# Kernel optimization log

Measured on AMD Instinct MI355X. Metric: run time of the kernel, lower is better.

The kernel has to match this reference:

```python
import jax, jax.numpy as jnp
import numpy as np

N = 50000   # nodes
E = 500000  # edges
G = 64      # graphs in batch
H = 2       # attention heads
D = 64      # hidden per head (hid)
F_IN = 4    # num_features
C = 5       # num_classes
NEG_SLOPE = 0.2


def setup_inputs() -> dict:
    key = jax.random.key(0)
    ks = jax.random.split(key, 24)
    inp = {
        'x': jax.random.normal(ks[0], (N, F_IN), jnp.float32),
        'edge_index': jax.random.randint(ks[1], (2, E), 0, N, dtype=jnp.int64),
        'batch': jnp.sort(jax.random.randint(ks[2], (N,), 0, G, dtype=jnp.int64)),
    }
    ins = [F_IN, H * D, H * D, H * D]
    ki = 3
    for l, fin in enumerate(ins, 1):
        s = 1.0 / np.sqrt(fin)
        inp[f'W{l}'] = s * jax.random.normal(ks[ki], (fin, H * D), jnp.float32); ki += 1
        inp[f'asrc{l}'] = 0.1 * jax.random.normal(ks[ki], (H, D), jnp.float32); ki += 1
        inp[f'adst{l}'] = 0.1 * jax.random.normal(ks[ki], (H, D), jnp.float32); ki += 1
        inp[f'b{l}'] = 0.01 * jax.random.normal(ks[ki], (H * D,), jnp.float32); ki += 1
    inp['lin_w'] = (1.0 / np.sqrt(H * D)) * jax.random.normal(ks[ki], (H * D, C), jnp.float32); ki += 1
    inp['lin_b'] = jnp.zeros((C,), jnp.float32)
    return inp


def gat_conv(x, src, dst, W, a_src, a_dst, b):
    # x: [N, Fin] -> h: [N, H, D]
    h = (x @ W).reshape(-1, H, D)
    alpha_src = jnp.sum(h * a_src, axis=-1)  # [N, H]
    alpha_dst = jnp.sum(h * a_dst, axis=-1)  # [N, H]
    e = jax.nn.leaky_relu(alpha_src[src] + alpha_dst[dst], NEG_SLOPE)  # [E, H]
    # segment softmax over incoming edges of each dst node
    e_max = jax.ops.segment_max(e, dst, num_segments=N)  # [N, H]
    e_exp = jnp.exp(e - e_max[dst])
    denom = jax.ops.segment_sum(e_exp, dst, num_segments=N)
    alpha = e_exp / (denom[dst] + 1e-16)  # [E, H]
    msg = h[src] * alpha[:, :, None]  # [E, H, D]
    out = jax.ops.segment_sum(msg, dst, num_segments=N)  # [N, H, D]
    return out.reshape(-1, H * D) + b


def reference(x, edge_index, batch,
              W1, asrc1, adst1, b1,
              W2, asrc2, adst2, b2,
              W3, asrc3, adst3, b3,
              W4, asrc4, adst4, b4,
              lin_w, lin_b):
    src, dst = edge_index[0], edge_index[1]
    h = jax.nn.relu(gat_conv(x, src, dst, W1, asrc1, adst1, b1))
    h = jax.nn.relu(gat_conv(h, src, dst, W2, asrc2, adst2, b2))
    h = jax.nn.relu(gat_conv(h, src, dst, W3, asrc3, adst3, b3))
    h = jax.nn.relu(gat_conv(h, src, dst, W4, asrc4, adst4, b4))
    # global mean pool over graphs
    sums = jax.ops.segment_sum(h, batch, num_segments=G)  # [G, 128]
    counts = jax.ops.segment_sum(jnp.ones((h.shape[0],), h.dtype), batch, num_segments=G)
    pooled = sums / jnp.maximum(counts, 1.0)[:, None]
    return jax.nn.sigmoid(pooled @ lin_w + lin_b)  # [G, C]
```

## Files before the change

kernel.cpp:

```cpp
#include <hip/hip_runtime.h>
#include <math.h>

#define NHEAD 2
#define NDIM  64
#define HD    128
#define NGRAPH 64
#define NCLS  5
#define NEG_SLOPE 0.2f

typedef __attribute__((ext_vector_type(8))) short bf16x8;
typedef __attribute__((ext_vector_type(4))) float f32x4;

static __device__ __forceinline__ unsigned short f2bf(float f) {
    unsigned int u = __float_as_uint(f);
    u = (u + 0x7fff + ((u >> 16) & 1)) >> 16;
    return (unsigned short)u;
}
static __device__ __forceinline__ float bf2f(unsigned short b) {
    return __uint_as_float((unsigned int)b << 16);
}


__global__ void k_deg(const int* __restrict__ dst, int* __restrict__ deg, int E) {
    int i = blockIdx.x * blockDim.x + threadIdx.x;
    if (i < E) atomicAdd(&deg[dst[i]], 1);
}

__global__ __launch_bounds__(256) void k_scan_local(const int* __restrict__ deg,
                                                    int* __restrict__ ptr,
                                                    int* __restrict__ bsum, int n) {
    __shared__ int wsum[4];
    const int tid = threadIdx.x, lane = tid & 63, wid = tid >> 6;
    const int base = blockIdx.x * 2048 + tid * 8;
    int v[8];
    #pragma unroll
    for (int k = 0; k < 8; ++k) {
        int i = base + k;
        v[k] = (i < n) ? deg[i] : 0;
    }
    #pragma unroll
    for (int k = 1; k < 8; ++k) v[k] += v[k - 1];
    int x = v[7];
    #pragma unroll
    for (int off = 1; off < 64; off <<= 1) {
        int t = __shfl_up(x, off, 64);
        if (lane >= off) x += t;
    }
    if (lane == 63) wsum[wid] = x;
    __syncthreads();
    int woff = 0;
    #pragma unroll
    for (int k = 0; k < 4; ++k) woff += (k < wid) ? wsum[k] : 0;
    int texcl = woff + x - v[7];
    #pragma unroll
    for (int k = 0; k < 8; ++k) {
        int i = base + k;
        if (i < n) ptr[i + 1] = texcl + v[k];
    }
    if (tid == 255) bsum[blockIdx.x] = woff + x;
    if (blockIdx.x == 0 && tid == 0) ptr[0] = 0;
}

__global__ void k_scan_bsum(int* __restrict__ bsum, int B) {
    int lane = threadIdx.x;
    int carry = 0;
    for (int base = 0; base < B; base += 64) {
        int i = base + lane;
        int v = (i < B) ? bsum[i] : 0;
        int x = v;
        #pragma unroll
        for (int off = 1; off < 64; off <<= 1) {
            int t = __shfl_up(x, off, 64);
            if (lane >= off) x += t;
        }
        if (i < B) bsum[i] = carry + x - v;
        carry += __shfl(x, 63, 64);
    }
}

__global__ __launch_bounds__(256) void k_scan_add(int* __restrict__ ptr,
                                                  const int* __restrict__ bsum, int n) {
    int off = bsum[blockIdx.x];
    if (off == 0) return;
    const int base = blockIdx.x * 2048 + threadIdx.x * 8;
    #pragma unroll
    for (int k = 0; k < 8; ++k) {
        int i = base + k;
        if (i < n) ptr[i + 1] += off;
    }
}

__global__ void k_scatter(const int* __restrict__ src, const int* __restrict__ dst,
                          const int* __restrict__ ptr, int* __restrict__ fill,
                          int* __restrict__ csr, int E) {
    int i = blockIdx.x * blockDim.x + threadIdx.x;
    if (i < E) {
        int d = dst[i];
        int pos = atomicAdd(&fill[d], 1);
        csr[ptr[d] + pos] = src[i];
    }
}


__global__ void k_prepw(const float* __restrict__ W2, const float* __restrict__ W3,
                        const float* __restrict__ W4, unsigned short* __restrict__ Wt) {
    int idx = blockIdx.x * blockDim.x + threadIdx.x;
    if (idx >= 3 * HD * HD) return;
    int l = idx / (HD * HD), rem = idx % (HD * HD);
    int n = rem >> 7, k = rem & 127;
    const float* W = (l == 0) ? W2 : (l == 1) ? W3 : W4;
    Wt[idx] = f2bf(W[k * HD + n]);
}

__global__ void k_gemm1_alpha(const float* __restrict__ x, const float* __restrict__ W,
                              const float* __restrict__ asrc, const float* __restrict__ adst,
                              unsigned short* __restrict__ out, float* __restrict__ oas,
                              float* __restrict__ oad, int N) {
    int n = (blockIdx.x * blockDim.x + threadIdx.x) >> 6;
    int lane = threadIdx.x & 63;
    if (n >= N) return;
    float4 xv = *(const float4*)&x[n * 4];
    int c0 = lane * 2;
    float2 w0 = *(const float2*)&W[c0];
    float2 w1 = *(const float2*)&W[128 + c0];
    float2 w2 = *(const float2*)&W[256 + c0];
    float2 w3 = *(const float2*)&W[384 + c0];
    float v0 = xv.x * w0.x + xv.y * w1.x + xv.z * w2.x + xv.w * w3.x;
    float v1 = xv.x * w0.y + xv.y * w1.y + xv.z * w2.y + xv.w * w3.y;
    unsigned short b0 = f2bf(v0), b1 = f2bf(v1);
    unsigned int packed = (unsigned int)b0 | ((unsigned int)b1 << 16);
    *(unsigned int*)&out[(size_t)n * HD + c0] = packed;
    float vx = bf2f(b0), vy = bf2f(b1);
    float2 av = *(const float2*)&asrc[c0];
    float2 dv = *(const float2*)&adst[c0];
    float s = vx * av.x + vy * av.y;
    float t = vx * dv.x + vy * dv.y;
    #pragma unroll
    for (int off = 16; off > 0; off >>= 1) {
        s += __shfl_xor(s, off);
        t += __shfl_xor(t, off);
    }
    if ((lane & 31) == 0) {
        int head = lane >> 5;
        oas[n * 2 + head] = s;
        oad[n * 2 + head] = t;
    }
}

__global__ __launch_bounds__(256) void k_gemm_mfma(const unsigned short* __restrict__ A,
                                                   const unsigned short* __restrict__ Wt,
                                                   const float* __restrict__ asrc,
                                                   const float* __restrict__ adst,
                                                   unsigned short* __restrict__ out,
                                                   float* __restrict__ oas,
                                                   float* __restrict__ oad, int N) {
    const int tid = threadIdx.x;
    const int nbase = blockIdx.x * 64;
    const int lane = tid & 63, w = tid >> 6;
    const int l15 = lane & 15, quad = lane >> 4;
    const int koff = quad * 8;

    float av[8], dv[8];
    #pragma unroll
    for (int c = 0; c < 8; ++c) {
        av[c] = asrc[c * 16 + l15];
        dv[c] = adst[c * 16 + l15];
    }

    f32x4 acc[8];
    #pragma unroll
    for (int c = 0; c < 8; ++c) acc[c] = (f32x4)(0.f);

    const int g0 = nbase + w * 16 + l15;
    #pragma unroll
    for (int ks = 0; ks < 4; ++ks) {
        bf16x8 a0 = (bf16x8)(short)0;
        if (g0 < N) a0 = *(const bf16x8*)&A[(size_t)g0 * HD + ks * 32 + koff];
        #pragma unroll
        for (int c = 0; c < 8; ++c) {
            bf16x8 b = *(const bf16x8*)&Wt[(size_t)(c * 16 + l15) * HD + ks * 32 + koff];
            acc[c] = __builtin_amdgcn_mfma_f32_16x16x32_bf16(a0, b, acc[c], 0, 0, 0);
        }
    }

    const int rowb = nbase + w * 16 + quad * 4;
    #pragma unroll
    for (int c = 0; c < 8; ++c) {
        f32x4 v = acc[c];
        int col = c * 16 + l15;
        #pragma unroll
        for (int r = 0; r < 4; ++r) {
            int row = rowb + r;
            if (row < N) out[(size_t)row * HD + col] = f2bf(v[r]);
        }
    }
    #pragma unroll
    for (int r = 0; r < 4; ++r) {
        float ps0 = 0.f, ps1 = 0.f, pd0 = 0.f, pd1 = 0.f;
        #pragma unroll
        for (int c = 0; c < 4; ++c) {
            float hv = acc[c][r];
            ps0 += hv * av[c]; pd0 += hv * dv[c];
        }
        #pragma unroll
        for (int c = 4; c < 8; ++c) {
            float hv = acc[c][r];
            ps1 += hv * av[c]; pd1 += hv * dv[c];
        }
        #pragma unroll
        for (int off = 1; off < 16; off <<= 1) {
            ps0 += __shfl_xor(ps0, off);
            ps1 += __shfl_xor(ps1, off);
            pd0 += __shfl_xor(pd0, off);
            pd1 += __shfl_xor(pd1, off);
        }
        int row = rowb + r;
        if (l15 == 0 && row < N) {
            *(float2*)&oas[row * 2] = make_float2(ps0, ps1);
            *(float2*)&oad[row * 2] = make_float2(pd0, pd1);
        }
    }
}

__global__ __launch_bounds__(256) void k_agg(const unsigned short* __restrict__ h,
                                             const float* __restrict__ oas,
                                             const float* __restrict__ oad,
                                             const int* __restrict__ ptr,
                                             const int* __restrict__ csr,
                                             const float* __restrict__ bias,
                                             unsigned short* __restrict__ out, int N) {
    const int tid = threadIdx.x;
    const int lane = tid & 63;
    const int grp = lane >> 4, sub = lane & 15;
    const int gbase = lane & 48;
    const int n = ((blockIdx.x * blockDim.x + tid) >> 6) * 4 + grp;
    const int hsel = sub >> 3;
    const bool valid = (n < N);

    int beg = 0, end = 0;
    float2 adn = make_float2(0.f, 0.f);
    if (valid) {
        beg = ptr[n]; end = ptr[n + 1];
        adn = *(const float2*)&oad[n * 2];
    }
    float m0 = -INFINITY, m1 = -INFINITY, l0 = 0.f, l1 = 0.f;
    float acc[8];
    #pragma unroll
    for (int k = 0; k < 8; ++k) acc[k] = 0.f;

    auto accum = [&](uint4 hv, float pj) {
        #pragma unroll
        for (int k = 0; k < 4; ++k) {
            unsigned int u = (&hv.x)[k];
            acc[2 * k]     += pj * __uint_as_float(u << 16);
            acc[2 * k + 1] += pj * __uint_as_float(u & 0xffff0000u);
        }
    };

    int cbeg = beg;
    while (__any(cbeg < end)) {
        int rem = end - cbeg;
        int cnt = rem < 0 ? 0 : (rem > 16 ? 16 : rem);
        int s = 0;
        float e0 = -INFINITY, e1 = -INFINITY;
        if (sub < cnt) {
            s = csr[cbeg + sub];
            float2 as = *(const float2*)&oas[s * 2];
            e0 = as.x + adn.x; e0 = (e0 >= 0.f) ? e0 : NEG_SLOPE * e0;
            e1 = as.y + adn.y; e1 = (e1 >= 0.f) ? e1 : NEG_SLOPE * e1;
        }
        float c0 = e0, c1 = e1;
        #pragma unroll
        for (int off = 8; off > 0; off >>= 1) {
            c0 = fmaxf(c0, __shfl_xor(c0, off));
            c1 = fmaxf(c1, __shfl_xor(c1, off));
        }
        float nm0 = fmaxf(m0, c0), nm1 = fmaxf(m1, c1);
        float sc0 = (nm0 == -INFINITY) ? 0.f : __expf(m0 - nm0);
        float sc1 = (nm1 == -INFINITY) ? 0.f : __expf(m1 - nm1);
        float p0 = (sub < cnt) ? __expf(e0 - nm0) : 0.f;
        float p1 = (sub < cnt) ? __expf(e1 - nm1) : 0.f;
        float s0 = p0, s1 = p1;
        #pragma unroll
        for (int off = 8; off > 0; off >>= 1) {
            s0 += __shfl_xor(s0, off);
            s1 += __shfl_xor(s1, off);
        }
        l0 = l0 * sc0 + s0;
        l1 = l1 * sc1 + s1;
        m0 = nm0; m1 = nm1;
        float scl = hsel ? sc1 : sc0;
        #pragma unroll
        for (int k = 0; k < 8; ++k) acc[k] *= scl;

        int jm = cnt;
        jm = max(jm, __shfl_xor(jm, 16));
        jm = max(jm, __shfl_xor(jm, 32));

        auto fetchp = [&](int j, uint4& hv, float& pj) {
            int sj = __shfl(s, gbase + j);
            float pa = __shfl(p0, gbase + j);
            float pb = __shfl(p1, gbase + j);
            pj = hsel ? pb : pa;
            hv = make_uint4(0, 0, 0, 0);
            if (j < cnt)
                hv = *(const uint4*)&h[(size_t)sj * HD + sub * 8];
        };
        uint4 hA, hB = make_uint4(0, 0, 0, 0);
        float pA, pB = 0.f;
        fetchp(0, hA, pA);
        if (jm > 1) fetchp(1, hB, pB);
        for (int j = 2; j < jm; ++j) {
            uint4 hC; float pC;
            fetchp(j, hC, pC);
            accum(hA, pA);
            hA = hB; pA = pB;
            hB = hC; pB = pC;
        }
        accum(hA, pA);
        if (jm > 1) accum(hB, pB);

        cbeg += 16;
    }

    if (valid) {
        float lsel = hsel ? l1 : l0;
        float inv = 1.f / (lsel + 1e-16f);
        float4 ba = *(const float4*)&bias[sub * 8];
        float4 bb = *(const float4*)&bias[sub * 8 + 4];
        float o[8];
        o[0] = fmaxf(acc[0] * inv + ba.x, 0.f);
        o[1] = fmaxf(acc[1] * inv + ba.y, 0.f);
        o[2] = fmaxf(acc[2] * inv + ba.z, 0.f);
        o[3] = fmaxf(acc[3] * inv + ba.w, 0.f);
        o[4] = fmaxf(acc[4] * inv + bb.x, 0.f);
        o[5] = fmaxf(acc[5] * inv + bb.y, 0.f);
        o[6] = fmaxf(acc[6] * inv + bb.z, 0.f);
        o[7] = fmaxf(acc[7] * inv + bb.w, 0.f);
        uint4 pk;
        pk.x = (unsigned int)f2bf(o[0]) | ((unsigned int)f2bf(o[1]) << 16);
        pk.y = (unsigned int)f2bf(o[2]) | ((unsigned int)f2bf(o[3]) << 16);
        pk.z = (unsigned int)f2bf(o[4]) | ((unsigned int)f2bf(o[5]) << 16);
        pk.w = (unsigned int)f2bf(o[6]) | ((unsigned int)f2bf(o[7]) << 16);
        *(uint4*)&out[(size_t)n * HD + sub * 8] = pk;
    }
}

__global__ void k_pool(const unsigned short* __restrict__ feat, const int* __restrict__ batch,
                       float* __restrict__ pooled, int* __restrict__ gcount, int N) {
    int col = threadIdx.x;
    int n0 = blockIdx.x * 128;
    int n1 = min(n0 + 128, N);
    float acc = 0.f;
    int curg = -1, runlen = 0;
    for (int n = n0; n < n1; ++n) {
        int g = batch[n];
        if (g != curg) {
            if (curg >= 0) {
                atomicAdd(&pooled[curg * HD + col], acc);
                if (col == 0) atomicAdd(&gcount[curg], runlen);
            }
            acc = 0.f; runlen = 0;
            curg = g;
        }
        acc += bf2f(feat[(size_t)n * HD + col]);
        runlen++;
    }
    if (curg >= 0) {
        atomicAdd(&pooled[curg * HD + col], acc);
        if (col == 0) atomicAdd(&gcount[curg], runlen);
    }
}

__global__ void k_final(const float* __restrict__ pooled, const int* __restrict__ gcount,
                        const float* __restrict__ lw, const float* __restrict__ lb,
                        float* __restrict__ out) {
    int tid = threadIdx.x;
    if (tid >= NGRAPH * NCLS) return;
    int g = tid / NCLS, c = tid % NCLS;
    float cnt = fmaxf((float)gcount[g], 1.f);
    const float* p = pooled + g * HD;
    float sum = 0.f;
    for (int k = 0; k < HD; ++k)
        sum += p[k] * lw[k * NCLS + c];
    float z = lb[c] + sum / cnt;
    out[tid] = 1.f / (1.f + __expf(-z));
}


static inline size_t al256(size_t x) { return (x + 255) & ~(size_t)255; }

extern "C" void kernel_launch(void* const* d_in, const int* in_sizes, int n_in,
                              void* d_out, int out_size, void* d_ws, size_t ws_size,
                              hipStream_t stream) {
    const int N = in_sizes[0] / 4;
    const int E = in_sizes[1] / 2;

    const float* x     = (const float*)d_in[0];
    const int*   esrc  = (const int*)d_in[1];
    const int*   edst  = esrc + E;
    const int*   batch = (const int*)d_in[2];
    const float* Wl[4]  = {(const float*)d_in[3],  (const float*)d_in[7],
                           (const float*)d_in[11], (const float*)d_in[15]};
    const float* asr[4] = {(const float*)d_in[4],  (const float*)d_in[8],
                           (const float*)d_in[12], (const float*)d_in[16]};
    const float* ads[4] = {(const float*)d_in[5],  (const float*)d_in[9],
                           (const float*)d_in[13], (const float*)d_in[17]};
    const float* bs[4]  = {(const float*)d_in[6],  (const float*)d_in[10],
                           (const float*)d_in[14], (const float*)d_in[18]};
    const float* lin_w = (const float*)d_in[19];
    const float* lin_b = (const float*)d_in[20];
    float* out = (float*)d_out;

    char* w = (char*)d_ws;
    size_t off = 0;
    auto alloc = [&](size_t bytes) -> void* {
        void* p = w + off;
        off = al256(off + bytes);
        return p;
    };
    int*   deg    = (int*)alloc((size_t)N * 4);
    int*   fill   = (int*)alloc((size_t)N * 4);
    int*   gcount = (int*)alloc((size_t)NGRAPH * 4);
    float* pooled = (float*)alloc((size_t)NGRAPH * HD * 4);
    size_t zbytes = off;
    int*   ptr    = (int*)alloc((size_t)(N + 1) * 4);
    int*   bsum   = (int*)alloc((size_t)1024 * 4);
    int*   csr    = (int*)alloc((size_t)E * 4);
    unsigned short* hbuf = (unsigned short*)alloc((size_t)N * HD * 2);
    unsigned short* feat = (unsigned short*)alloc((size_t)N * HD * 2);
    unsigned short* Wt   = (unsigned short*)alloc((size_t)3 * HD * HD * 2);
    float* a_src  = (float*)alloc((size_t)N * 2 * 4);
    float* a_dst  = (float*)alloc((size_t)N * 2 * 4);
    (void)ws_size; (void)n_in; (void)out_size;

    hipMemsetAsync(d_ws, 0, zbytes, stream);

    k_prepw<<<(3 * HD * HD + 255) / 256, 256, 0, stream>>>(Wl[1], Wl[2], Wl[3], Wt);
    k_deg<<<(E + 255) / 256, 256, 0, stream>>>(edst, deg, E);
    const int SB = (N + 2047) / 2048;
    k_scan_local<<<SB, 256, 0, stream>>>(deg, ptr, bsum, N);
    k_scan_bsum<<<1, 64, 0, stream>>>(bsum, SB);
    k_scan_add<<<SB, 256, 0, stream>>>(ptr, bsum, N);
    k_scatter<<<(E + 255) / 256, 256, 0, stream>>>(esrc, edst, ptr, fill, csr, E);

    const int node_wave_blocks = (N + 3) / 4;
    const int agg_blocks = (N + 15) / 16;

    for (int layer = 0; layer < 4; ++layer) {
        if (layer == 0) {
            k_gemm1_alpha<<<node_wave_blocks, 256, 0, stream>>>(
                x, Wl[0], asr[0], ads[0], hbuf, a_src, a_dst, N);
        } else {
            k_gemm_mfma<<<(N + 63) / 64, 256, 0, stream>>>(
                feat, Wt + (size_t)(layer - 1) * HD * HD,
                asr[layer], ads[layer], hbuf, a_src, a_dst, N);
        }
        k_agg<<<agg_blocks, 256, 0, stream>>>(hbuf, a_src, a_dst, ptr, csr, bs[layer], feat, N);
    }

    k_pool<<<(N + 127) / 128, 128, 0, stream>>>(feat, batch, pooled, gcount, N);
    k_final<<<1, 320, 0, stream>>>(pooled, gcount, lin_w, lin_b, out);
}
```

Baseline: 396.1 us.

## Fuse GAT aggregation with next layer's MFMA projection via LDS tile

Merges each layer's edge aggregation kernel with the following layer's bf16 MFMA projection and attention-logit computation. Aggregated rows are staged in a padded shared-memory tile instead of being written to and re-read from global memory. Ping-pong buffers for h and the alpha arrays keep reads and writes apart across layers. This removes three kernel launches and the intermediate feature round trip, but each block now runs 4 sequential aggregation passes before its GEMM, which lowers parallelism in the gather phase.

```diff
diff --git a/kernel.cpp b/kernel.cpp
--- a/kernel.cpp
+++ b/kernel.cpp
@@ -7,6 +7,7 @@
 #define NGRAPH 64
 #define NCLS  5
 #define NEG_SLOPE 0.2f
+#define LDA 136
 
 typedef __attribute__((ext_vector_type(8))) short bf16x8;
 typedef __attribute__((ext_vector_type(4))) float f32x4;
@@ -147,96 +148,12 @@
     }
 }
 
-__global__ __launch_bounds__(256) void k_gemm_mfma(const unsigned short* __restrict__ A,
-                                                   const unsigned short* __restrict__ Wt,
-                                                   const float* __restrict__ asrc,
-                                                   const float* __restrict__ adst,
-                                                   unsigned short* __restrict__ out,
-                                                   float* __restrict__ oas,
-                                                   float* __restrict__ oad, int N) {
-    const int tid = threadIdx.x;
-    const int nbase = blockIdx.x * 64;
-    const int lane = tid & 63, w = tid >> 6;
-    const int l15 = lane & 15, quad = lane >> 4;
-    const int koff = quad * 8;
-
-    float av[8], dv[8];
-    #pragma unroll
-    for (int c = 0; c < 8; ++c) {
-        av[c] = asrc[c * 16 + l15];
-        dv[c] = adst[c * 16 + l15];
-    }
-
-    f32x4 acc[8];
-    #pragma unroll
-    for (int c = 0; c < 8; ++c) acc[c] = (f32x4)(0.f);
-
-    const int g0 = nbase + w * 16 + l15;
-    #pragma unroll
-    for (int ks = 0; ks < 4; ++ks) {
-        bf16x8 a0 = (bf16x8)(short)0;
-        if (g0 < N) a0 = *(const bf16x8*)&A[(size_t)g0 * HD + ks * 32 + koff];
-        #pragma unroll
-        for (int c = 0; c < 8; ++c) {
-            bf16x8 b = *(const bf16x8*)&Wt[(size_t)(c * 16 + l15) * HD + ks * 32 + koff];
-            acc[c] = __builtin_amdgcn_mfma_f32_16x16x32_bf16(a0, b, acc[c], 0, 0, 0);
-        }
-    }
-
-    const int rowb = nbase + w * 16 + quad * 4;
-    #pragma unroll
-    for (int c = 0; c < 8; ++c) {
-        f32x4 v = acc[c];
-        int col = c * 16 + l15;
-        #pragma unroll
-        for (int r = 0; r < 4; ++r) {
-            int row = rowb + r;
-            if (row < N) out[(size_t)row * HD + col] = f2bf(v[r]);
-        }
-    }
-    #pragma unroll
-    for (int r = 0; r < 4; ++r) {
-        float ps0 = 0.f, ps1 = 0.f, pd0 = 0.f, pd1 = 0.f;
-        #pragma unroll
-        for (int c = 0; c < 4; ++c) {
-            float hv = acc[c][r];
-            ps0 += hv * av[c]; pd0 += hv * dv[c];
-        }
-        #pragma unroll
-        for (int c = 4; c < 8; ++c) {
-            float hv = acc[c][r];
-            ps1 += hv * av[c]; pd1 += hv * dv[c];
-        }
-        #pragma unroll
-        for (int off = 1; off < 16; off <<= 1) {
-            ps0 += __shfl_xor(ps0, off);
-            ps1 += __shfl_xor(ps1, off);
-            pd0 += __shfl_xor(pd0, off);
-            pd1 += __shfl_xor(pd1, off);
-        }
-        int row = rowb + r;
-        if (l15 == 0 && row < N) {
-            *(float2*)&oas[row * 2] = make_float2(ps0, ps1);
-            *(float2*)&oad[row * 2] = make_float2(pd0, pd1);
-        }
-    }
-}
-
-__global__ __launch_bounds__(256) void k_agg(const unsigned short* __restrict__ h,
-                                             const float* __restrict__ oas,
-                                             const float* __restrict__ oad,
-                                             const int* __restrict__ ptr,
-                                             const int* __restrict__ csr,
-                                             const float* __restrict__ bias,
-                                             unsigned short* __restrict__ out, int N) {
-    const int tid = threadIdx.x;
-    const int lane = tid & 63;
-    const int grp = lane >> 4, sub = lane & 15;
-    const int gbase = lane & 48;
-    const int n = ((blockIdx.x * blockDim.x + tid) >> 6) * 4 + grp;
-    const int hsel = sub >> 3;
+static __device__ __forceinline__ uint4 agg_row(
+    const unsigned short* __restrict__ h, const float* __restrict__ oas,
+    const float* __restrict__ oad, const int* __restrict__ ptr,
+    const int* __restrict__ csr, const float* __restrict__ bias,
+    int n, int N, int sub, int gbase, int hsel) {
     const bool valid = (n < N);
-
     int beg = 0, end = 0;
     float2 adn = make_float2(0.f, 0.f);
     if (valid) {
@@ -323,6 +240,7 @@
         cbeg += 16;
     }
 
+    uint4 pk = make_uint4(0, 0, 0, 0);
     if (valid) {
         float lsel = hsel ? l1 : l0;
         float inv = 1.f / (lsel + 1e-16f);
@@ -337,13 +255,113 @@
         o[5] = fmaxf(acc[5] * inv + bb.y, 0.f);
         o[6] = fmaxf(acc[6] * inv + bb.z, 0.f);
         o[7] = fmaxf(acc[7] * inv + bb.w, 0.f);
-        uint4 pk;
         pk.x = (unsigned int)f2bf(o[0]) | ((unsigned int)f2bf(o[1]) << 16);
         pk.y = (unsigned int)f2bf(o[2]) | ((unsigned int)f2bf(o[3]) << 16);
         pk.z = (unsigned int)f2bf(o[4]) | ((unsigned int)f2bf(o[5]) << 16);
         pk.w = (unsigned int)f2bf(o[6]) | ((unsigned int)f2bf(o[7]) << 16);
-        *(uint4*)&out[(size_t)n * HD + sub * 8] = pk;
-    }
+    }
+    return pk;
+}
+
+__global__ __launch_bounds__(256) void k_agg_gemm(
+    const unsigned short* __restrict__ hin,
+    const float* __restrict__ oas_in, const float* __restrict__ oad_in,
+    const int* __restrict__ ptr, const int* __restrict__ csr,
+    const float* __restrict__ bias,
+    const unsigned short* __restrict__ Wt,
+    const float* __restrict__ asrc, const float* __restrict__ adst,
+    unsigned short* __restrict__ hout,
+    float* __restrict__ oas_out, float* __restrict__ oad_out, int N) {
+    __shared__ unsigned short As[64 * LDA];
+    const int tid = threadIdx.x;
+    const int lane = tid & 63, w = tid >> 6;
+    const int grp = lane >> 4, sub = lane & 15;
+    const int gbase = lane & 48;
+    const int hsel = sub >> 3;
+    const int nbase = blockIdx.x * 64;
+
+    #pragma unroll 1
+    for (int p = 0; p < 4; ++p) {
+        const int row = w * 16 + p * 4 + grp;
+        uint4 pk = agg_row(hin, oas_in, oad_in, ptr, csr, bias,
+                           nbase + row, N, sub, gbase, hsel);
+        *(uint4*)&As[(size_t)row * LDA + sub * 8] = pk;
+    }
+    __syncthreads();
+
+    float av[8], dv[8];
+    #pragma unroll
+    for (int c = 0; c < 8; ++c) {
+        av[c] = asrc[c * 16 + sub];
+        dv[c] = adst[c * 16 + sub];
+    }
+    f32x4 acc[8];
+    #pragma unroll
+    for (int c = 0; c < 8; ++c) acc[c] = (f32x4)(0.f);
+
+    #pragma unroll
+    for (int ks = 0; ks < 4; ++ks) {
+        bf16x8 a0 = *(const bf16x8*)&As[(size_t)(w * 16 + sub) * LDA + ks * 32 + grp * 8];
+        #pragma unroll
+        for (int c = 0; c < 8; ++c) {
+            bf16x8 b = *(const bf16x8*)&Wt[(size_t)(c * 16 + sub) * HD + ks * 32 + grp * 8];
+            acc[c] = __builtin_amdgcn_mfma_f32_16x16x32_bf16(a0, b, acc[c], 0, 0, 0);
+        }
+    }
+
+    const int rowb = nbase + w * 16 + grp * 4;
+    #pragma unroll
+    for (int c = 0; c < 8; ++c) {
+        f32x4 v = acc[c];
+        int col = c * 16 + sub;
+        #pragma unroll
+        for (int r = 0; r < 4; ++r) {
+            int row = rowb + r;
+            if (row < N) hout[(size_t)row * HD + col] = f2bf(v[r]);
+        }
+    }
+    #pragma unroll
+    for (int r = 0; r < 4; ++r) {
+        float ps0 = 0.f, ps1 = 0.f, pd0 = 0.f, pd1 = 0.f;
+        #pragma unroll
+        for (int c = 0; c < 4; ++c) {
+            float hv = acc[c][r];
+            ps0 += hv * av[c]; pd0 += hv * dv[c];
+        }
+        #pragma unroll
+        for (int c = 4; c < 8; ++c) {
+            float hv = acc[c][r];
+            ps1 += hv * av[c]; pd1 += hv * dv[c];
+        }
+        #pragma unroll
+        for (int off = 1; off < 16; off <<= 1) {
+            ps0 += __shfl_xor(ps0, off);
+            ps1 += __shfl_xor(ps1, off);
+            pd0 += __shfl_xor(pd0, off);
+            pd1 += __shfl_xor(pd1, off);
+        }
+        int row = rowb + r;
+        if (sub == 0 && row < N) {
+            *(float2*)&oas_out[row * 2] = make_float2(ps0, ps1);
+            *(float2*)&oad_out[row * 2] = make_float2(pd0, pd1);
+        }
+    }
+}
+
+__global__ __launch_bounds__(256) void k_agg_final(
+    const unsigned short* __restrict__ hin,
+    const float* __restrict__ oas_in, const float* __restrict__ oad_in,
+    const int* __restrict__ ptr, const int* __restrict__ csr,
+    const float* __restrict__ bias,
+    unsigned short* __restrict__ out, int N) {
+    const int tid = threadIdx.x;
+    const int lane = tid & 63;
+    const int grp = lane >> 4, sub = lane & 15;
+    const int gbase = lane & 48;
+    const int hsel = sub >> 3;
+    const int n = ((blockIdx.x * blockDim.x + tid) >> 6) * 4 + grp;
+    uint4 pk = agg_row(hin, oas_in, oad_in, ptr, csr, bias, n, N, sub, gbase, hsel);
+    if (n < N) *(uint4*)&out[(size_t)n * HD + sub * 8] = pk;
 }
 
 __global__ void k_pool(const unsigned short* __restrict__ feat, const int* __restrict__ batch,
@@ -427,11 +445,14 @@
     int*   ptr    = (int*)alloc((size_t)(N + 1) * 4);
     int*   bsum   = (int*)alloc((size_t)1024 * 4);
     int*   csr    = (int*)alloc((size_t)E * 4);
-    unsigned short* hbuf = (unsigned short*)alloc((size_t)N * HD * 2);
+    unsigned short* hA   = (unsigned short*)alloc((size_t)N * HD * 2);
+    unsigned short* hB   = (unsigned short*)alloc((size_t)N * HD * 2);
     unsigned short* feat = (unsigned short*)alloc((size_t)N * HD * 2);
     unsigned short* Wt   = (unsigned short*)alloc((size_t)3 * HD * HD * 2);
-    float* a_src  = (float*)alloc((size_t)N * 2 * 4);
-    float* a_dst  = (float*)alloc((size_t)N * 2 * 4);
+    float* asA = (float*)alloc((size_t)N * 2 * 4);
+    float* adA = (float*)alloc((size_t)N * 2 * 4);
+    float* asB = (float*)alloc((size_t)N * 2 * 4);
+    float* adB = (float*)alloc((size_t)N * 2 * 4);
     (void)ws_size; (void)n_in; (void)out_size;
 
     hipMemsetAsync(d_ws, 0, zbytes, stream);
@@ -444,20 +465,21 @@
     k_scan_add<<<SB, 256, 0, stream>>>(ptr, bsum, N);
     k_scatter<<<(E + 255) / 256, 256, 0, stream>>>(esrc, edst, ptr, fill, csr, E);
 
-    const int node_wave_blocks = (N + 3) / 4;
-    const int agg_blocks = (N + 15) / 16;
-
-    for (int layer = 0; layer < 4; ++layer) {
-        if (layer == 0) {
-            k_gemm1_alpha<<<node_wave_blocks, 256, 0, stream>>>(
-                x, Wl[0], asr[0], ads[0], hbuf, a_src, a_dst, N);
-        } else {
-            k_gemm_mfma<<<(N + 63) / 64, 256, 0, stream>>>(
-                feat, Wt + (size_t)(layer - 1) * HD * HD,
-                asr[layer], ads[layer], hbuf, a_src, a_dst, N);
-        }
-        k_agg<<<agg_blocks, 256, 0, stream>>>(hbuf, a_src, a_dst, ptr, csr, bs[layer], feat, N);
-    }
+    const int fused_blocks = (N + 63) / 64;
+
+    k_gemm1_alpha<<<(N + 3) / 4, 256, 0, stream>>>(
+        x, Wl[0], asr[0], ads[0], hA, asA, adA, N);
+    k_agg_gemm<<<fused_blocks, 256, 0, stream>>>(
+        hA, asA, adA, ptr, csr, bs[0], Wt,
+        asr[1], ads[1], hB, asB, adB, N);
+    k_agg_gemm<<<fused_blocks, 256, 0, stream>>>(
+        hB, asB, adB, ptr, csr, bs[1], Wt + (size_t)HD * HD,
+        asr[2], ads[2], hA, asA, adA, N);
+    k_agg_gemm<<<fused_blocks, 256, 0, stream>>>(
+        hA, asA, adA, ptr, csr, bs[2], Wt + (size_t)2 * HD * HD,
+        asr[3], ads[3], hB, asB, adB, N);
+    k_agg_final<<<(N + 15) / 16, 256, 0, stream>>>(
+        hB, asB, adB, ptr, csr, bs[3], feat, N);
 
     k_pool<<<(N + 127) / 128, 128, 0, stream>>>(feat, batch, pooled, gcount, N);
     k_final<<<1, 320, 0, stream>>>(pooled, gcount, lin_w, lin_b, out);
```

Measured after the change: 390.5 us. No clear change (-1.4%).

## Split GAT aggregation into edge-exp, node-sum and quarter-column gather kernels

Applied to the files above, without the earlier changes.

Replaces the fused online-softmax aggregation kernel with three passes. A per-edge kernel computes the exp of the attention score, a per-node kernel sums those values into an inverse denominator, and a gather kernel walks the CSR over quarter-column planes (32 bf16 per node). Features are stored as four 32-column planes so each gather pass touches a smaller working set, which is meant to improve cache hit rates. The trade-off is extra kernel launches and extra traffic for the edge exp array and the dst array. It also drops max subtraction in favour of clamping the score at 80, which changes numerics for large scores.

```diff
diff --git a/kernel.cpp b/kernel.cpp
--- a/kernel.cpp
+++ b/kernel.cpp
@@ -92,12 +92,14 @@
 
 __global__ void k_scatter(const int* __restrict__ src, const int* __restrict__ dst,
                           const int* __restrict__ ptr, int* __restrict__ fill,
-                          int* __restrict__ csr, int E) {
+                          int* __restrict__ csr, int* __restrict__ dstE, int E) {
     int i = blockIdx.x * blockDim.x + threadIdx.x;
     if (i < E) {
         int d = dst[i];
         int pos = atomicAdd(&fill[d], 1);
-        csr[ptr[d] + pos] = src[i];
+        int slot = ptr[d] + pos;
+        csr[slot] = src[i];
+        dstE[slot] = d;
     }
 }
 
@@ -114,8 +116,9 @@
 
 __global__ void k_gemm1_alpha(const float* __restrict__ x, const float* __restrict__ W,
                               const float* __restrict__ asrc, const float* __restrict__ adst,
-                              unsigned short* __restrict__ out, float* __restrict__ oas,
+                              unsigned short* __restrict__ hq, float* __restrict__ oas,
                               float* __restrict__ oad, int N) {
+    const size_t NS = (size_t)N * 32;
     int n = (blockIdx.x * blockDim.x + threadIdx.x) >> 6;
     int lane = threadIdx.x & 63;
     if (n >= N) return;
@@ -129,16 +132,18 @@
     float v1 = xv.x * w0.y + xv.y * w1.y + xv.z * w2.y + xv.w * w3.y;
     unsigned short b0 = f2bf(v0), b1 = f2bf(v1);
     unsigned int packed = (unsigned int)b0 | ((unsigned int)b1 << 16);
-    *(unsigned int*)&out[(size_t)n * HD + c0] = packed;
+    int p = lane >> 4;
+    int off = c0 & 31;
+    *(unsigned int*)&hq[(size_t)p * NS + (size_t)n * 32 + off] = packed;
     float vx = bf2f(b0), vy = bf2f(b1);
     float2 av = *(const float2*)&asrc[c0];
     float2 dv = *(const float2*)&adst[c0];
     float s = vx * av.x + vy * av.y;
     float t = vx * dv.x + vy * dv.y;
     #pragma unroll
-    for (int off = 16; off > 0; off >>= 1) {
-        s += __shfl_xor(s, off);
-        t += __shfl_xor(t, off);
+    for (int off2 = 16; off2 > 0; off2 >>= 1) {
+        s += __shfl_xor(s, off2);
+        t += __shfl_xor(t, off2);
     }
     if ((lane & 31) == 0) {
         int head = lane >> 5;
@@ -147,13 +152,100 @@
     }
 }
 
-__global__ __launch_bounds__(256) void k_gemm_mfma(const unsigned short* __restrict__ A,
-                                                   const unsigned short* __restrict__ Wt,
-                                                   const float* __restrict__ asrc,
-                                                   const float* __restrict__ adst,
-                                                   unsigned short* __restrict__ out,
-                                                   float* __restrict__ oas,
-                                                   float* __restrict__ oad, int N) {
+__global__ void k_edge_exp(const int* __restrict__ csr, const int* __restrict__ dstE,
+                           const float* __restrict__ oas, const float* __restrict__ oad,
+                           float* __restrict__ expE, int E) {
+    int i = blockIdx.x * blockDim.x + threadIdx.x;
+    if (i >= E) return;
+    int s = csr[i], d = dstE[i];
+    float2 as = *(const float2*)&oas[s * 2];
+    float2 ad = *(const float2*)&oad[d * 2];
+    float e0 = as.x + ad.x; e0 = (e0 >= 0.f) ? e0 : NEG_SLOPE * e0;
+    float e1 = as.y + ad.y; e1 = (e1 >= 0.f) ? e1 : NEG_SLOPE * e1;
+    e0 = fminf(e0, 80.f); e1 = fminf(e1, 80.f);
+    *(float2*)&expE[(size_t)i * 2] = make_float2(__expf(e0), __expf(e1));
+}
+
+__global__ __launch_bounds__(256) void k_node_inv(const int* __restrict__ ptr,
+                                                  const float* __restrict__ expE,
+                                                  float* __restrict__ invL, int N) {
+    int t = blockIdx.x * blockDim.x + threadIdx.x;
+    int n = t >> 2, l4 = t & 3;
+    if (n >= N) return;
+    int beg = ptr[n], end = ptr[n + 1];
+    float s0 = 0.f, s1 = 0.f;
+    for (int j = beg + l4; j < end; j += 4) {
+        float2 p = *(const float2*)&expE[(size_t)j * 2];
+        s0 += p.x; s1 += p.y;
+    }
+    s0 += __shfl_xor(s0, 1); s0 += __shfl_xor(s0, 2);
+    s1 += __shfl_xor(s1, 1); s1 += __shfl_xor(s1, 2);
+    if (l4 == 0)
+        *(float2*)&invL[n * 2] = make_float2(1.f / (s0 + 1e-16f), 1.f / (s1 + 1e-16f));
+}
+
+__global__ __launch_bounds__(256) void k_gather_q(
+    const unsigned short* __restrict__ hin,
+    const float* __restrict__ expE, const float* __restrict__ invL,
+    const int* __restrict__ ptr, const int* __restrict__ csr,
+    const float* __restrict__ bias,
+    unsigned short* __restrict__ out_q,
+    unsigned short* __restrict__ out_rm,
+    int rowmajor, int N) {
+    const size_t NS = (size_t)N * 32;
+    const int q = blockIdx.y;
+    const int t = threadIdx.x >> 2, l4 = threadIdx.x & 3;
+    const int n = blockIdx.x * 64 + t;
+    if (n >= N) return;
+    const int head = q >> 1;
+    const int beg = ptr[n], end = ptr[n + 1];
+    const float inv = invL[n * 2 + head];
+    const unsigned short* __restrict__ hp = hin + (size_t)q * NS;
+    float acc[8];
+    #pragma unroll
+    for (int k = 0; k < 8; ++k) acc[k] = 0.f;
+    for (int j = beg; j < end; ++j) {
+        int s = __builtin_nontemporal_load(&csr[j]);
+        float pe = __builtin_nontemporal_load(&expE[(size_t)j * 2 + head]);
+        float a = pe * inv;
+        uint4 hv = *(const uint4*)&hp[(size_t)s * 32 + l4 * 8];
+        #pragma unroll
+        for (int k = 0; k < 4; ++k) {
+            unsigned int u = (&hv.x)[k];
+            acc[2 * k]     += a * __uint_as_float(u << 16);
+            acc[2 * k + 1] += a * __uint_as_float(u & 0xffff0000u);
+        }
+    }
+    const int dimb = q * 32 + l4 * 8;
+    float4 ba = *(const float4*)&bias[dimb];
+    float4 bb = *(const float4*)&bias[dimb + 4];
+    float o[8];
+    o[0] = fmaxf(acc[0] + ba.x, 0.f);
+    o[1] = fmaxf(acc[1] + ba.y, 0.f);
+    o[2] = fmaxf(acc[2] + ba.z, 0.f);
+    o[3] = fmaxf(acc[3] + ba.w, 0.f);
+    o[4] = fmaxf(acc[4] + bb.x, 0.f);
+    o[5] = fmaxf(acc[5] + bb.y, 0.f);
+    o[6] = fmaxf(acc[6] + bb.z, 0.f);
+    o[7] = fmaxf(acc[7] + bb.w, 0.f);
+    uint4 pk;
+    pk.x = (unsigned int)f2bf(o[0]) | ((unsigned int)f2bf(o[1]) << 16);
+    pk.y = (unsigned int)f2bf(o[2]) | ((unsigned int)f2bf(o[3]) << 16);
+    pk.z = (unsigned int)f2bf(o[4]) | ((unsigned int)f2bf(o[5]) << 16);
+    pk.w = (unsigned int)f2bf(o[6]) | ((unsigned int)f2bf(o[7]) << 16);
+    if (rowmajor)
+        *(uint4*)&out_rm[(size_t)n * HD + dimb] = pk;
+    else
+        *(uint4*)&out_q[(size_t)q * NS + (size_t)n * 32 + l4 * 8] = pk;
+}
+
+__global__ __launch_bounds__(256) void k_gemm_mfma(
+    const unsigned short* __restrict__ Aq,
+    const unsigned short* __restrict__ Wt,
+    const float* __restrict__ asrc, const float* __restrict__ adst,
+    unsigned short* __restrict__ hq_out,
+    float* __restrict__ oas, float* __restrict__ oad, int N) {
+    const size_t NS = (size_t)N * 32;
     const int tid = threadIdx.x;
     const int nbase = blockIdx.x * 64;
     const int lane = tid & 63, w = tid >> 6;
@@ -175,7 +267,7 @@
     #pragma unroll
     for (int ks = 0; ks < 4; ++ks) {
         bf16x8 a0 = (bf16x8)(short)0;
-        if (g0 < N) a0 = *(const bf16x8*)&A[(size_t)g0 * HD + ks * 32 + koff];
+        if (g0 < N) a0 = *(const bf16x8*)&Aq[(size_t)ks * NS + (size_t)g0 * 32 + koff];
         #pragma unroll
         for (int c = 0; c < 8; ++c) {
             bf16x8 b = *(const bf16x8*)&Wt[(size_t)(c * 16 + l15) * HD + ks * 32 + koff];
@@ -187,11 +279,12 @@
     #pragma unroll
     for (int c = 0; c < 8; ++c) {
         f32x4 v = acc[c];
-        int col = c * 16 + l15;
+        const int p = c >> 1;
+        const int coff = (c & 1) * 16 + l15;
         #pragma unroll
         for (int r = 0; r < 4; ++r) {
             int row = rowb + r;
-            if (row < N) out[(size_t)row * HD + col] = f2bf(v[r]);
+            if (row < N) hq_out[(size_t)p * NS + (size_t)row * 32 + coff] = f2bf(v[r]);
         }
     }
     #pragma unroll
@@ -219,130 +312,6 @@
             *(float2*)&oas[row * 2] = make_float2(ps0, ps1);
             *(float2*)&oad[row * 2] = make_float2(pd0, pd1);
         }
-    }
-}
-
-__global__ __launch_bounds__(256) void k_agg(const unsigned short* __restrict__ h,
-                                             const float* __restrict__ oas,
-                                             const float* __restrict__ oad,
-                                             const int* __restrict__ ptr,
-                                             const int* __restrict__ csr,
-                                             const float* __restrict__ bias,
-                                             unsigned short* __restrict__ out, int N) {
-    const int tid = threadIdx.x;
-    const int lane = tid & 63;
-    const int grp = lane >> 4, sub = lane & 15;
-    const int gbase = lane & 48;
-    const int n = ((blockIdx.x * blockDim.x + tid) >> 6) * 4 + grp;
-    const int hsel = sub >> 3;
-    const bool valid = (n < N);
-
-    int beg = 0, end = 0;
-    float2 adn = make_float2(0.f, 0.f);
-    if (valid) {
-        beg = ptr[n]; end = ptr[n + 1];
-        adn = *(const float2*)&oad[n * 2];
-    }
-    float m0 = -INFINITY, m1 = -INFINITY, l0 = 0.f, l1 = 0.f;
-    float acc[8];
-    #pragma unroll
-    for (int k = 0; k < 8; ++k) acc[k] = 0.f;
-
-    auto accum = [&](uint4 hv, float pj) {
-        #pragma unroll
-        for (int k = 0; k < 4; ++k) {
-            unsigned int u = (&hv.x)[k];
-            acc[2 * k]     += pj * __uint_as_float(u << 16);
-            acc[2 * k + 1] += pj * __uint_as_float(u & 0xffff0000u);
-        }
-    };
-
-    int cbeg = beg;
-    while (__any(cbeg < end)) {
-        int rem = end - cbeg;
-        int cnt = rem < 0 ? 0 : (rem > 16 ? 16 : rem);
-        int s = 0;
-        float e0 = -INFINITY, e1 = -INFINITY;
-        if (sub < cnt) {
-            s = csr[cbeg + sub];
-            float2 as = *(const float2*)&oas[s * 2];
-            e0 = as.x + adn.x; e0 = (e0 >= 0.f) ? e0 : NEG_SLOPE * e0;
-            e1 = as.y + adn.y; e1 = (e1 >= 0.f) ? e1 : NEG_SLOPE * e1;
-        }
-        float c0 = e0, c1 = e1;
-        #pragma unroll
-        for (int off = 8; off > 0; off >>= 1) {
-            c0 = fmaxf(c0, __shfl_xor(c0, off));
-            c1 = fmaxf(c1, __shfl_xor(c1, off));
-        }
-        float nm0 = fmaxf(m0, c0), nm1 = fmaxf(m1, c1);
-        float sc0 = (nm0 == -INFINITY) ? 0.f : __expf(m0 - nm0);
-        float sc1 = (nm1 == -INFINITY) ? 0.f : __expf(m1 - nm1);
-        float p0 = (sub < cnt) ? __expf(e0 - nm0) : 0.f;
-        float p1 = (sub < cnt) ? __expf(e1 - nm1) : 0.f;
-        float s0 = p0, s1 = p1;
-        #pragma unroll
-        for (int off = 8; off > 0; off >>= 1) {
-            s0 += __shfl_xor(s0, off);
-            s1 += __shfl_xor(s1, off);
-        }
-        l0 = l0 * sc0 + s0;
-        l1 = l1 * sc1 + s1;
-        m0 = nm0; m1 = nm1;
-        float scl = hsel ? sc1 : sc0;
-        #pragma unroll
-        for (int k = 0; k < 8; ++k) acc[k] *= scl;
-
-        int jm = cnt;
-        jm = max(jm, __shfl_xor(jm, 16));
-        jm = max(jm, __shfl_xor(jm, 32));
-
-        auto fetchp = [&](int j, uint4& hv, float& pj) {
-            int sj = __shfl(s, gbase + j);
-            float pa = __shfl(p0, gbase + j);
-            float pb = __shfl(p1, gbase + j);
-            pj = hsel ? pb : pa;
-            hv = make_uint4(0, 0, 0, 0);
-            if (j < cnt)
-                hv = *(const uint4*)&h[(size_t)sj * HD + sub * 8];
-        };
-        uint4 hA, hB = make_uint4(0, 0, 0, 0);
-        float pA, pB = 0.f;
-        fetchp(0, hA, pA);
-        if (jm > 1) fetchp(1, hB, pB);
-        for (int j = 2; j < jm; ++j) {
-            uint4 hC; float pC;
-            fetchp(j, hC, pC);
-            accum(hA, pA);
-            hA = hB; pA = pB;
-            hB = hC; pB = pC;
-        }
-        accum(hA, pA);
-        if (jm > 1) accum(hB, pB);
-
-        cbeg += 16;
-    }
-
-    if (valid) {
-        float lsel = hsel ? l1 : l0;
-        float inv = 1.f / (lsel + 1e-16f);
-        float4 ba = *(const float4*)&bias[sub * 8];
-        float4 bb = *(const float4*)&bias[sub * 8 + 4];
-        float o[8];
-        o[0] = fmaxf(acc[0] * inv + ba.x, 0.f);
-        o[1] = fmaxf(acc[1] * inv + ba.y, 0.f);
-        o[2] = fmaxf(acc[2] * inv + ba.z, 0.f);
-        o[3] = fmaxf(acc[3] * inv + ba.w, 0.f);
-        o[4] = fmaxf(acc[4] * inv + bb.x, 0.f);
-        o[5] = fmaxf(acc[5] * inv + bb.y, 0.f);
-        o[6] = fmaxf(acc[6] * inv + bb.z, 0.f);
-        o[7] = fmaxf(acc[7] * inv + bb.w, 0.f);
-        uint4 pk;
-        pk.x = (unsigned int)f2bf(o[0]) | ((unsigned int)f2bf(o[1]) << 16);
-        pk.y = (unsigned int)f2bf(o[2]) | ((unsigned int)f2bf(o[3]) << 16);
-        pk.z = (unsigned int)f2bf(o[4]) | ((unsigned int)f2bf(o[5]) << 16);
-        pk.w = (unsigned int)f2bf(o[6]) | ((unsigned int)f2bf(o[7]) << 16);
-        *(uint4*)&out[(size_t)n * HD + sub * 8] = pk;
     }
 }
 
@@ -427,11 +396,17 @@
     int*   ptr    = (int*)alloc((size_t)(N + 1) * 4);
     int*   bsum   = (int*)alloc((size_t)1024 * 4);
     int*   csr    = (int*)alloc((size_t)E * 4);
-    unsigned short* hbuf = (unsigned short*)alloc((size_t)N * HD * 2);
+    int*   dstE   = (int*)alloc((size_t)E * 4);
+    float* expE   = (float*)alloc((size_t)E * 2 * 4);
+    float* invL   = (float*)alloc((size_t)N * 2 * 4);
+    unsigned short* P1   = (unsigned short*)alloc((size_t)N * HD * 2);
+    unsigned short* P2   = (unsigned short*)alloc((size_t)N * HD * 2);
     unsigned short* feat = (unsigned short*)alloc((size_t)N * HD * 2);
     unsigned short* Wt   = (unsigned short*)alloc((size_t)3 * HD * HD * 2);
-    float* a_src  = (float*)alloc((size_t)N * 2 * 4);
-    float* a_dst  = (float*)alloc((size_t)N * 2 * 4);
+    float* asA = (float*)alloc((size_t)N * 2 * 4);
+    float* adA = (float*)alloc((size_t)N * 2 * 4);
+    float* asB = (float*)alloc((size_t)N * 2 * 4);
+    float* adB = (float*)alloc((size_t)N * 2 * 4);
     (void)ws_size; (void)n_in; (void)out_size;
 
     hipMemsetAsync(d_ws, 0, zbytes, stream);
@@ -442,21 +417,32 @@
     k_scan_local<<<SB, 256, 0, stream>>>(deg, ptr, bsum, N);
     k_scan_bsum<<<1, 64, 0, stream>>>(bsum, SB);
     k_scan_add<<<SB, 256, 0, stream>>>(ptr, bsum, N);
-    k_scatter<<<(E + 255) / 256, 256, 0, stream>>>(esrc, edst, ptr, fill, csr, E);
-
-    const int node_wave_blocks = (N + 3) / 4;
-    const int agg_blocks = (N + 15) / 16;
-
-    for (int layer = 0; layer < 4; ++layer) {
-        if (layer == 0) {
-            k_gemm1_alpha<<<node_wave_blocks, 256, 0, stream>>>(
-                x, Wl[0], asr[0], ads[0], hbuf, a_src, a_dst, N);
+    k_scatter<<<(E + 255) / 256, 256, 0, stream>>>(esrc, edst, ptr, fill, csr, dstE, E);
+
+    const int eblk = (E + 255) / 256;
+    const int tblk = (N * 4 + 255) / 256;
+    const dim3 gq((N + 63) / 64, 4);
+
+    k_gemm1_alpha<<<(N + 3) / 4, 256, 0, stream>>>(
+        x, Wl[0], asr[0], ads[0], P1, asA, adA, N);
+
+    const float* cas = asA; const float* cad = adA;
+    float* nas = asB;       float* nad = adB;
+    for (int i = 0; i < 4; ++i) {
+        k_edge_exp<<<eblk, 256, 0, stream>>>(csr, dstE, cas, cad, expE, E);
+        k_node_inv<<<tblk, 256, 0, stream>>>(ptr, expE, invL, N);
+        if (i < 3) {
+            k_gather_q<<<gq, 256, 0, stream>>>(
+                P1, expE, invL, ptr, csr, bs[i], P2, (unsigned short*)nullptr, 0, N);
+            k_gemm_mfma<<<(N + 63) / 64, 256, 0, stream>>>(
+                P2, Wt + (size_t)i * HD * HD, asr[i + 1], ads[i + 1],
+                P1, nas, nad, N);
+            const float* ts = cas; cas = nas; nas = (float*)ts;
+            const float* td = cad; cad = nad; nad = (float*)td;
         } else {
-            k_gemm_mfma<<<(N + 63) / 64, 256, 0, stream>>>(
-                feat, Wt + (size_t)(layer - 1) * HD * HD,
-                asr[layer], ads[layer], hbuf, a_src, a_dst, N);
-        }
-        k_agg<<<agg_blocks, 256, 0, stream>>>(hbuf, a_src, a_dst, ptr, csr, bs[layer], feat, N);
+            k_gather_q<<<gq, 256, 0, stream>>>(
+                P1, expE, invL, ptr, csr, bs[i], (unsigned short*)nullptr, feat, 1, N);
+        }
     }
 
     k_pool<<<(N + 127) / 128, 128, 0, stream>>>(feat, batch, pooled, gcount, N);
```

New measurement: 606.3 us. +53.1%, slower.
